# Performance work log

Measured on AMD Instinct MI355X. Metric: run time of the kernel, lower is better.

## Reference

```python
import jax, jax.numpy as jnp
import numpy as np

NUM_EMBEDDINGS = 16384
EMBED_DIM = 256
COMMITMENT_COST = 0.25  # legacy=True: vq_loss = commit + beta * codebook


def setup_inputs() -> dict:
    key = jax.random.key(0)
    k1, k2, k3, k4 = jax.random.split(key, 4)
    z = jax.random.normal(k1, (8, 2048, EMBED_DIM), dtype=jnp.float32)
    # frozen codebook: normal(0, embedding_dim ** -0.5)
    codebook = jax.random.normal(k2, (NUM_EMBEDDINGS, EMBED_DIM), dtype=jnp.float32) * (EMBED_DIM ** -0.5)
    # learnable linear projection, torch default uniform init
    bound = 1.0 / np.sqrt(EMBED_DIM)
    proj_w = jax.random.uniform(k3, (EMBED_DIM, EMBED_DIM), dtype=jnp.float32, minval=-bound, maxval=bound)
    proj_b = jax.random.uniform(k4, (EMBED_DIM,), dtype=jnp.float32, minval=-bound, maxval=bound)
    return {"z": z, "codebook": codebook, "proj_w": proj_w, "proj_b": proj_b}


def reference(z, codebook, proj_w, proj_b):
    B, T, D = z.shape
    # projected codebook (the only learned part of the quantizer)
    quant_codebook = codebook @ proj_w.T + proj_b  # [K, D]
    z_flat = z.reshape(-1, D)  # [N, D]
    # squared L2 distances: ||z||^2 + ||c||^2 - 2 z.c
    dists = (
        jnp.sum(z_flat * z_flat, axis=1, keepdims=True)
        + jnp.sum(quant_codebook * quant_codebook, axis=1)
        - 2.0 * jnp.einsum("nd,kd->nk", z_flat, quant_codebook)
    )  # [N, K]
    idx = jnp.argmin(dists, axis=1)  # [N]
    quantized = quant_codebook[idx].reshape(z.shape)  # [B, T, D]

    commitment_loss = jnp.mean((jax.lax.stop_gradient(quantized) - z) ** 2)
    codebook_loss = jnp.mean((quantized - jax.lax.stop_gradient(z)) ** 2)
    vq_loss = commitment_loss + COMMITMENT_COST * codebook_loss  # legacy formulation

    # straight-through estimator
    quantized = z + jax.lax.stop_gradient(quantized - z)
    encoding_indices = idx.reshape(B, T)
    return quantized, vq_loss, encoding_indices
```

## Files before the change

### kernel.cpp

```cpp
#include <hip/hip_runtime.h>

typedef unsigned short u16;
typedef __bf16 bf16x8 __attribute__((ext_vector_type(8)));
typedef float f32x4 __attribute__((ext_vector_type(4)));

#define NQ 16384
#define NC 16384
#define DD 256
#define BM 256
#define BN 256
#define BK 32
#define NSPLIT 8
#define NPART (NSPLIT * 2)
#define NTILES ((NC / NSPLIT) / BN)
#define NSTEPS (NTILES * 8)

__device__ __forceinline__ u16 f2bf(float x) {
  unsigned u = __float_as_uint(x);
  u += 0x7fffu + ((u >> 16) & 1u);
  return (u16)(u >> 16);
}
__device__ __forceinline__ float bf2f(u16 h) {
  return __uint_as_float(((unsigned)h) << 16);
}

__device__ __forceinline__ void gl2lds16(const void* g, void* l) {
  __builtin_amdgcn_global_load_lds((__attribute__((address_space(1))) void*)g,
                                   (__attribute__((address_space(3))) void*)l,
                                   16, 0, 0);
}

#define MFMA_AGPR(ACC, A, B) \
  asm("v_mfma_f32_16x16x32_bf16 %0, %1, %2, %0" : "+a"(ACC) : "v"(A), "v"(B))

__global__ __launch_bounds__(256) void split_z_kernel(const float* __restrict__ z,
                                                      u16* __restrict__ Ah,
                                                      u16* __restrict__ Al) {
  size_t i = (size_t)blockIdx.x * 256 + threadIdx.x;
  float4 v = ((const float4*)z)[i];
  float f[4] = {v.x, v.y, v.z, v.w};
  u16 hh[4], ll[4];
#pragma unroll
  for (int j = 0; j < 4; ++j) {
    hh[j] = f2bf(f[j]);
    ll[j] = f2bf(f[j] - bf2f(hh[j]));
  }
  ushort4 h; h.x = hh[0]; h.y = hh[1]; h.z = hh[2]; h.w = hh[3];
  ushort4 l; l.x = ll[0]; l.y = ll[1]; l.z = ll[2]; l.w = ll[3];
  ((ushort4*)Ah)[i] = h;
  ((ushort4*)Al)[i] = l;
}

__global__ __launch_bounds__(256) void norm_both_kernel(const float* __restrict__ z,
                                                        const float* __restrict__ qc,
                                                        float* __restrict__ zn,
                                                        float* __restrict__ cn) {
  const int t = threadIdx.x;
  const int j = t & 7;
  const bool isq = blockIdx.x >= (NQ / 32);
  const int b = isq ? (blockIdx.x - NQ / 32) : blockIdx.x;
  const float* x = isq ? qc : z;
  float* nrm = isq ? cn : zn;
  const int row = b * 32 + (t >> 3);
  const float* q = x + (size_t)row * 256;
  float half[2];
#pragma unroll
  for (int h = 0; h < 2; ++h) {
    const float* p = q + h * 128;
    float v0 = p[j];
    float r = __fmul_rn(v0, v0);
#pragma unroll
    for (int i = 8; i < 128; i += 8) {
      float v = p[i + j];
      r = __fadd_rn(r, __fmul_rn(v, v));
    }
    float s1 = __fadd_rn(r, __shfl_xor(r, 1));
    float s2 = __fadd_rn(s1, __shfl_xor(s1, 2));
    half[h] = __fadd_rn(s2, __shfl_xor(s2, 4));
  }
  if (j == 0) nrm[row] = __fadd_rn(half[0], half[1]);
}

__global__ __launch_bounds__(256) void qc_gemm_kernel(const float* __restrict__ cb,
                                                      const float* __restrict__ W,
                                                      const float* __restrict__ bias,
                                                      float* __restrict__ qc,
                                                      u16* __restrict__ Bh,
                                                      u16* __restrict__ Bl) {
  __shared__ float As[64][33];
  __shared__ float Bs[64][33];
  const int bm = blockIdx.x >> 2;
  const int bn = blockIdx.x & 3;
  const int m0 = bm * 64, n0 = bn * 64;
  const int t = threadIdx.x;
  const int tx = t & 15, ty = t >> 4;
  float acc[4][4] = {};
  for (int kc = 0; kc < 256; kc += 32) {
    __syncthreads();
#pragma unroll
    for (int j = 0; j < 8; ++j) {
      int idx = j * 256 + t;
      int r = idx >> 5, c = idx & 31;
      As[r][c] = cb[(size_t)(m0 + r) * 256 + kc + c];
      Bs[r][c] = W[(size_t)(n0 + r) * 256 + kc + c];
    }
    __syncthreads();
#pragma unroll
    for (int kk = 0; kk < 32; ++kk) {
      float a[4], b[4];
#pragma unroll
      for (int u = 0; u < 4; ++u) a[u] = As[ty * 4 + u][kk];
#pragma unroll
      for (int v = 0; v < 4; ++v) b[v] = Bs[tx * 4 + v][kk];
#pragma unroll
      for (int u = 0; u < 4; ++u)
#pragma unroll
        for (int v = 0; v < 4; ++v) acc[u][v] += a[u] * b[v];
    }
  }
#pragma unroll
  for (int u = 0; u < 4; ++u) {
    const int r = m0 + ty * 4 + u;
    const int c0 = n0 + tx * 4;
    float q4[4];
#pragma unroll
    for (int v = 0; v < 4; ++v) q4[v] = acc[u][v] + bias[c0 + v];
    float4 qv; qv.x = q4[0]; qv.y = q4[1]; qv.z = q4[2]; qv.w = q4[3];
    *(float4*)&qc[(size_t)r * 256 + c0] = qv;
    u16 hh[4], ll[4];
#pragma unroll
    for (int v = 0; v < 4; ++v) {
      hh[v] = f2bf(q4[v]);
      ll[v] = f2bf(q4[v] - bf2f(hh[v]));
    }
    ushort4 h; h.x = hh[0]; h.y = hh[1]; h.z = hh[2]; h.w = hh[3];
    ushort4 l; l.x = ll[0]; l.y = ll[1]; l.z = ll[2]; l.w = ll[3];
    *(ushort4*)&Bh[(size_t)r * 256 + c0] = h;
    *(ushort4*)&Bl[(size_t)r * 256 + c0] = l;
  }
}

__global__ __launch_bounds__(512, 2) void vq_argmin_kernel(
    const u16* __restrict__ Ah, const u16* __restrict__ Al,
    const u16* __restrict__ Bh, const u16* __restrict__ Bl,
    const float* __restrict__ cnorm, const float* __restrict__ znorm,
    float* __restrict__ pval, int* __restrict__ pidx) {
  __shared__ __align__(16) u16 Ahs[2][BM * BK];
  __shared__ __align__(16) u16 Als[2][BM * BK];
  __shared__ __align__(16) u16 Bhs[2][BN * BK];
  __shared__ __align__(16) u16 Bls[2][BN * BK];

  const int bm = blockIdx.x / NSPLIT;
  const int spl = blockIdx.x % NSPLIT;
  const int lane = threadIdx.x & 63;
  const int wid = threadIdx.x >> 6;
  const int wm = wid >> 1, wn = wid & 1;
  const int l15 = lane & 15;
  const int lg = lane >> 4;
  const int m0 = bm * BM;
  const int ns0 = spl * (NC / NSPLIT);

  const int st_r = lane >> 2;
  const int st_k = (((lane & 3) ^ ((lane >> 3) & 3)) << 3);

  const int rd_sw = ((lg ^ ((l15 >> 1) & 3)) << 3);

  const int grp0 = wid * 2, grp1 = wid * 2 + 1;
  const int stoff0 = (grp0 * 16 + st_r) * DD + st_k;
  const int stoff1 = (grp1 * 16 + st_r) * DD + st_k;
  const int dst0 = grp0 * 512, dst1 = grp1 * 512;

  auto stage = [&](int buf, int s2) {
    const int kcc = (s2 & 7) * BK;
    const u16* pAh = Ah + (size_t)m0 * DD + kcc;
    const u16* pAl = Al + (size_t)m0 * DD + kcc;
    const size_t bb = (size_t)(ns0 + (s2 >> 3) * BN) * DD + kcc;
    const u16* pBh = Bh + bb;
    const u16* pBl = Bl + bb;
    gl2lds16(pAh + stoff0, &Ahs[buf][dst0]);
    gl2lds16(pAl + stoff0, &Als[buf][dst0]);
    gl2lds16(pBh + stoff0, &Bhs[buf][dst0]);
    gl2lds16(pBl + stoff0, &Bls[buf][dst0]);
    gl2lds16(pAh + stoff1, &Ahs[buf][dst1]);
    gl2lds16(pAl + stoff1, &Als[buf][dst1]);
    gl2lds16(pBh + stoff1, &Bhs[buf][dst1]);
    gl2lds16(pBl + stoff1, &Bls[buf][dst1]);
  };

  float rmin[4][4];
  int ridx[4][4];
#pragma unroll
  for (int a = 0; a < 4; ++a)
#pragma unroll
    for (int b = 0; b < 4; ++b) { rmin[a][b] = 3.4e38f; ridx[a][b] = 0; }

  stage(0, 0);
  asm volatile("s_waitcnt vmcnt(0)" ::: "memory");
  __builtin_amdgcn_s_barrier();

  for (int nt = 0; nt < NTILES; ++nt) {
    const int n0 = ns0 + nt * BN;
    f32x4 acc[4][8];
#pragma unroll
    for (int a = 0; a < 4; ++a)
#pragma unroll
      for (int b = 0; b < 8; ++b) {
        f32x4 zz = {0.f, 0.f, 0.f, 0.f};
        acc[a][b] = zz;
      }

#pragma unroll 1
    for (int k8 = 0; k8 < 8; ++k8) {
      const int s = nt * 8 + k8;
      const int cur = s & 1;

      __builtin_amdgcn_s_barrier();
      if (s + 1 < NSTEPS) {
        stage(cur ^ 1, s + 1);
        asm volatile("s_waitcnt vmcnt(8)" ::: "memory");
      } else {
        asm volatile("s_waitcnt vmcnt(0)" ::: "memory");
      }
      __builtin_amdgcn_s_barrier();
      __builtin_amdgcn_sched_barrier(0);

      bf16x8 ah[4], al[4];
#pragma unroll
      for (int mi = 0; mi < 4; ++mi) {
        const int r = wm * 64 + mi * 16 + l15;
        const int off = r * BK + rd_sw;
        ah[mi] = *(const bf16x8*)&Ahs[cur][off];
        al[mi] = *(const bf16x8*)&Als[cur][off];
      }
      __builtin_amdgcn_s_setprio(1);
      {
        bf16x8 bh[4], bl[4];
#pragma unroll
        for (int nq = 0; nq < 4; ++nq) {
          const int r = wn * 128 + nq * 16 + l15;
          const int off = r * BK + rd_sw;
          bh[nq] = *(const bf16x8*)&Bhs[cur][off];
          bl[nq] = *(const bf16x8*)&Bls[cur][off];
        }
#pragma unroll
        for (int nq = 0; nq < 4; ++nq)
#pragma unroll
          for (int mi = 0; mi < 4; ++mi)
            MFMA_AGPR(acc[mi][nq], ah[mi], bh[nq]);
#pragma unroll
        for (int nq = 0; nq < 4; ++nq)
#pragma unroll
          for (int mi = 0; mi < 4; ++mi)
            MFMA_AGPR(acc[mi][nq], ah[mi], bl[nq]);
#pragma unroll
        for (int nq = 0; nq < 4; ++nq)
#pragma unroll
          for (int mi = 0; mi < 4; ++mi)
            MFMA_AGPR(acc[mi][nq], al[mi], bh[nq]);
      }
      __builtin_amdgcn_sched_barrier(0);
      {
        bf16x8 bh[4], bl[4];
#pragma unroll
        for (int nq = 0; nq < 4; ++nq) {
          const int r = wn * 128 + (4 + nq) * 16 + l15;
          const int off = r * BK + rd_sw;
          bh[nq] = *(const bf16x8*)&Bhs[cur][off];
          bl[nq] = *(const bf16x8*)&Bls[cur][off];
        }
#pragma unroll
        for (int nq = 0; nq < 4; ++nq)
#pragma unroll
          for (int mi = 0; mi < 4; ++mi)
            MFMA_AGPR(acc[mi][4 + nq], ah[mi], bh[nq]);
#pragma unroll
        for (int nq = 0; nq < 4; ++nq)
#pragma unroll
          for (int mi = 0; mi < 4; ++mi)
            MFMA_AGPR(acc[mi][4 + nq], ah[mi], bl[nq]);
#pragma unroll
        for (int nq = 0; nq < 4; ++nq)
#pragma unroll
          for (int mi = 0; mi < 4; ++mi)
            MFMA_AGPR(acc[mi][4 + nq], al[mi], bh[nq]);
      }
      __builtin_amdgcn_s_setprio(0);
    }

    float cnv[8];
#pragma unroll
    for (int ni = 0; ni < 8; ++ni)
      cnv[ni] = cnorm[n0 + wn * 128 + ni * 16 + l15];
#pragma unroll
    for (int mi = 0; mi < 4; ++mi) {
      float zr[4];
#pragma unroll
      for (int i = 0; i < 4; ++i)
        zr[i] = znorm[m0 + wm * 64 + mi * 16 + lg * 4 + i];
#pragma unroll
      for (int ni = 0; ni < 8; ++ni) {
        const int col = n0 + wn * 128 + ni * 16 + l15;
        const float cn = cnv[ni];
#pragma unroll
        for (int i = 0; i < 4; ++i) {
          const float s = __fadd_rn(zr[i], cn);
          const float v = __fsub_rn(s, __fmul_rn(2.0f, acc[mi][ni][i]));
          if (v < rmin[mi][i]) { rmin[mi][i] = v; ridx[mi][i] = col; }
        }
      }
    }
  }
#pragma unroll
  for (int mi = 0; mi < 4; ++mi)
#pragma unroll
    for (int i = 0; i < 4; ++i) {
      float v = rmin[mi][i];
      int ix = ridx[mi][i];
#pragma unroll
      for (int d = 1; d < 16; d <<= 1) {
        float ov = __shfl_xor(v, d);
        int oi = __shfl_xor(ix, d);
        if (ov < v || (ov == v && oi < ix)) { v = ov; ix = oi; }
      }
      if (l15 == 0) {
        const int row = m0 + wm * 64 + mi * 16 + lg * 4 + i;
        const int part = spl * 2 + wn;
        pval[(size_t)part * NQ + row] = v;
        pidx[(size_t)part * NQ + row] = ix;
      }
    }
}

__global__ __launch_bounds__(256) void finalize_kernel(
    const float* __restrict__ pval, const int* __restrict__ pidx,
    const float* __restrict__ qc, const float* __restrict__ z,
    float* __restrict__ out, float* __restrict__ loss_acc) {
  __shared__ int sidx[8];
  __shared__ float red[256];
  const int bid = blockIdx.x;
  const int t = threadIdx.x;
  if (t < 8) {
    const int row = bid * 8 + t;
    float best = pval[row];
    int bi = pidx[row];
    for (int s2 = 1; s2 < NPART; ++s2) {
      float v = pval[(size_t)s2 * NQ + row];
      int ix = pidx[(size_t)s2 * NQ + row];
      if (v < best || (v == best && ix < bi)) { best = v; bi = ix; }
    }
    sidx[t] = bi;
    out[4194305 + row] = (float)bi;
  }
  __syncthreads();
  float d2 = 0.f;
#pragma unroll
  for (int r = 0; r < 8; ++r) {
    const int row = bid * 8 + r;
    const int ix = sidx[r];
    const float q = qc[(size_t)ix * 256 + t];
    const float zz = z[(size_t)row * 256 + t];
    out[(size_t)row * 256 + t] = q;
    const float d = q - zz;
    d2 += d * d;
  }
  red[t] = d2;
  for (int st = 128; st; st >>= 1) {
    __syncthreads();
    if (t < st) red[t] += red[t + st];
  }
  if (t == 0) atomicAdd(loss_acc, red[0]);
}

__global__ void write_loss_kernel(const float* __restrict__ loss_acc, float* __restrict__ out) {
  out[4194304] = 1.25f * loss_acc[0] / 4194304.0f;
}

extern "C" void kernel_launch(void* const* d_in, const int* in_sizes, int n_in,
                              void* d_out, int out_size, void* d_ws, size_t ws_size,
                              hipStream_t stream) {
  const float* z = (const float*)d_in[0];
  const float* cb = (const float*)d_in[1];
  const float* W = (const float*)d_in[2];
  const float* bias = (const float*)d_in[3];
  float* out = (float*)d_out;
  char* ws = (char*)d_ws;

  constexpr size_t OFF_QC = 0;
  constexpr size_t OFF_AH = OFF_QC + 16777216;
  constexpr size_t OFF_AL = OFF_AH + 8388608;
  constexpr size_t OFF_BH = OFF_AL + 8388608;
  constexpr size_t OFF_BL = OFF_BH + 8388608;
  constexpr size_t OFF_CN = OFF_BL + 8388608;
  constexpr size_t OFF_ZN = OFF_CN + 65536;
  constexpr size_t OFF_PV = OFF_ZN + 65536;
  constexpr size_t OFF_PI = OFF_PV + 1048576;
  constexpr size_t OFF_ACC = OFF_PI + 1048576;

  float* qc = (float*)(ws + OFF_QC);
  u16* Ah = (u16*)(ws + OFF_AH);
  u16* Al = (u16*)(ws + OFF_AL);
  u16* Bh = (u16*)(ws + OFF_BH);
  u16* Bl = (u16*)(ws + OFF_BL);
  float* cn = (float*)(ws + OFF_CN);
  float* zn = (float*)(ws + OFF_ZN);
  float* pv = (float*)(ws + OFF_PV);
  int* pi = (int*)(ws + OFF_PI);
  float* lacc = (float*)(ws + OFF_ACC);

  hipMemsetAsync(lacc, 0, 4, stream);
  split_z_kernel<<<4096, 256, 0, stream>>>(z, Ah, Al);
  qc_gemm_kernel<<<1024, 256, 0, stream>>>(cb, W, bias, qc, Bh, Bl);
  norm_both_kernel<<<NQ / 32 + NC / 32, 256, 0, stream>>>(z, qc, zn, cn);
  vq_argmin_kernel<<<(NQ / BM) * NSPLIT, 512, 0, stream>>>(Ah, Al, Bh, Bl, cn, zn, pv, pi);
  finalize_kernel<<<NQ / 8, 256, 0, stream>>>(pv, pi, qc, z, out, lacc);
  write_loss_kernel<<<1, 1, 0, stream>>>(lacc, out);
}
```

Before: 522.8 us.

## Fuse z split with z-norm and enlarge codebook projection GEMM tiles

Merges the z bf16 hi/lo split with the z row-norm computation: z is staged in shared memory and read once from global memory instead of twice. The codebook projection GEMM moves from 64x64 tiles with 4x4 per-thread outputs to 128x128 tiles with 8x8 per-thread outputs and transposed LDS layout, so it can use vectorized float4 shared loads and do more arithmetic per load. The larger tile uses more registers and launches only 256 blocks, which may reduce occupancy. These preprocessing kernels are small next to the main argmin kernel.

```diff
diff --git a/kernel.cpp b/kernel.cpp
--- a/kernel.cpp
+++ b/kernel.cpp
@@ -33,35 +33,58 @@
 #define MFMA_AGPR(ACC, A, B) \
   asm("v_mfma_f32_16x16x32_bf16 %0, %1, %2, %0" : "+a"(ACC) : "v"(A), "v"(B))
 
-__global__ __launch_bounds__(256) void split_z_kernel(const float* __restrict__ z,
-                                                      u16* __restrict__ Ah,
-                                                      u16* __restrict__ Al) {
-  size_t i = (size_t)blockIdx.x * 256 + threadIdx.x;
-  float4 v = ((const float4*)z)[i];
-  float f[4] = {v.x, v.y, v.z, v.w};
-  u16 hh[4], ll[4];
-#pragma unroll
-  for (int j = 0; j < 4; ++j) {
-    hh[j] = f2bf(f[j]);
-    ll[j] = f2bf(f[j] - bf2f(hh[j]));
-  }
-  ushort4 h; h.x = hh[0]; h.y = hh[1]; h.z = hh[2]; h.w = hh[3];
-  ushort4 l; l.x = ll[0]; l.y = ll[1]; l.z = ll[2]; l.w = ll[3];
-  ((ushort4*)Ah)[i] = h;
-  ((ushort4*)Al)[i] = l;
-}
-
-__global__ __launch_bounds__(256) void norm_both_kernel(const float* __restrict__ z,
-                                                        const float* __restrict__ qc,
-                                                        float* __restrict__ zn,
-                                                        float* __restrict__ cn) {
+__global__ __launch_bounds__(256) void split_z_norm_kernel(const float* __restrict__ z,
+                                                           u16* __restrict__ Ah,
+                                                           u16* __restrict__ Al,
+                                                           float* __restrict__ zn) {
+  __shared__ float zs[32 * 256];
+  const int t = threadIdx.x;
+#pragma unroll
+  for (int j = 0; j < 8; ++j) {
+    const int loc = j * 256 + t;
+    const size_t i = (size_t)blockIdx.x * 2048 + loc;
+    float4 v = ((const float4*)z)[i];
+    *(float4*)&zs[loc * 4] = v;
+    float f[4] = {v.x, v.y, v.z, v.w};
+    u16 hh[4], ll[4];
+#pragma unroll
+    for (int q = 0; q < 4; ++q) {
+      hh[q] = f2bf(f[q]);
+      ll[q] = f2bf(f[q] - bf2f(hh[q]));
+    }
+    ushort4 h; h.x = hh[0]; h.y = hh[1]; h.z = hh[2]; h.w = hh[3];
+    ushort4 l; l.x = ll[0]; l.y = ll[1]; l.z = ll[2]; l.w = ll[3];
+    ((ushort4*)Ah)[i] = h;
+    ((ushort4*)Al)[i] = l;
+  }
+  __syncthreads();
+  const int j = t & 7;
+  const int lrow = t >> 3;
+  const int row = blockIdx.x * 32 + lrow;
+  const float* q = zs + lrow * 256;
+  float half[2];
+#pragma unroll
+  for (int h = 0; h < 2; ++h) {
+    const float* p = q + h * 128;
+    float v0 = p[j];
+    float r = __fmul_rn(v0, v0);
+#pragma unroll
+    for (int i = 8; i < 128; i += 8) {
+      float v = p[i + j];
+      r = __fadd_rn(r, __fmul_rn(v, v));
+    }
+    float s1 = __fadd_rn(r, __shfl_xor(r, 1));
+    float s2 = __fadd_rn(s1, __shfl_xor(s1, 2));
+    half[h] = __fadd_rn(s2, __shfl_xor(s2, 4));
+  }
+  if (j == 0) zn[row] = __fadd_rn(half[0], half[1]);
+}
+
+__global__ __launch_bounds__(256) void norm256_kernel(const float* __restrict__ x,
+                                                      float* __restrict__ nrm) {
   const int t = threadIdx.x;
   const int j = t & 7;
-  const bool isq = blockIdx.x >= (NQ / 32);
-  const int b = isq ? (blockIdx.x - NQ / 32) : blockIdx.x;
-  const float* x = isq ? qc : z;
-  float* nrm = isq ? cn : zn;
-  const int row = b * 32 + (t >> 3);
+  const int row = blockIdx.x * 32 + (t >> 3);
   const float* q = x + (size_t)row * 256;
   float half[2];
 #pragma unroll
@@ -87,56 +110,60 @@
                                                       float* __restrict__ qc,
                                                       u16* __restrict__ Bh,
                                                       u16* __restrict__ Bl) {
-  __shared__ float As[64][33];
-  __shared__ float Bs[64][33];
-  const int bm = blockIdx.x >> 2;
-  const int bn = blockIdx.x & 3;
-  const int m0 = bm * 64, n0 = bn * 64;
+  __shared__ float At[32][132];
+  __shared__ float Bt[32][132];
+  const int bm = blockIdx.x >> 1;
+  const int bn = blockIdx.x & 1;
+  const int m0 = bm * 128, n0 = bn * 128;
   const int t = threadIdx.x;
   const int tx = t & 15, ty = t >> 4;
-  float acc[4][4] = {};
+  float acc[8][8] = {};
   for (int kc = 0; kc < 256; kc += 32) {
     __syncthreads();
 #pragma unroll
-    for (int j = 0; j < 8; ++j) {
-      int idx = j * 256 + t;
-      int r = idx >> 5, c = idx & 31;
-      As[r][c] = cb[(size_t)(m0 + r) * 256 + kc + c];
-      Bs[r][c] = W[(size_t)(n0 + r) * 256 + kc + c];
+    for (int j = 0; j < 16; ++j) {
+      const int idx = j * 256 + t;
+      const int r = idx >> 5, c = idx & 31;
+      At[c][r] = cb[(size_t)(m0 + r) * 256 + kc + c];
+      Bt[c][r] = W[(size_t)(n0 + r) * 256 + kc + c];
     }
     __syncthreads();
 #pragma unroll
     for (int kk = 0; kk < 32; ++kk) {
-      float a[4], b[4];
-#pragma unroll
-      for (int u = 0; u < 4; ++u) a[u] = As[ty * 4 + u][kk];
-#pragma unroll
-      for (int v = 0; v < 4; ++v) b[v] = Bs[tx * 4 + v][kk];
-#pragma unroll
-      for (int u = 0; u < 4; ++u)
-#pragma unroll
-        for (int v = 0; v < 4; ++v) acc[u][v] += a[u] * b[v];
-    }
-  }
-#pragma unroll
-  for (int u = 0; u < 4; ++u) {
-    const int r = m0 + ty * 4 + u;
-    const int c0 = n0 + tx * 4;
-    float q4[4];
-#pragma unroll
-    for (int v = 0; v < 4; ++v) q4[v] = acc[u][v] + bias[c0 + v];
-    float4 qv; qv.x = q4[0]; qv.y = q4[1]; qv.z = q4[2]; qv.w = q4[3];
-    *(float4*)&qc[(size_t)r * 256 + c0] = qv;
-    u16 hh[4], ll[4];
-#pragma unroll
-    for (int v = 0; v < 4; ++v) {
-      hh[v] = f2bf(q4[v]);
-      ll[v] = f2bf(q4[v] - bf2f(hh[v]));
-    }
-    ushort4 h; h.x = hh[0]; h.y = hh[1]; h.z = hh[2]; h.w = hh[3];
-    ushort4 l; l.x = ll[0]; l.y = ll[1]; l.z = ll[2]; l.w = ll[3];
-    *(ushort4*)&Bh[(size_t)r * 256 + c0] = h;
-    *(ushort4*)&Bl[(size_t)r * 256 + c0] = l;
+      float4 a0 = *(const float4*)&At[kk][ty * 8];
+      float4 a1 = *(const float4*)&At[kk][ty * 8 + 4];
+      float4 b0 = *(const float4*)&Bt[kk][tx * 8];
+      float4 b1 = *(const float4*)&Bt[kk][tx * 8 + 4];
+      float a[8] = {a0.x, a0.y, a0.z, a0.w, a1.x, a1.y, a1.z, a1.w};
+      float b[8] = {b0.x, b0.y, b0.z, b0.w, b1.x, b1.y, b1.z, b1.w};
+#pragma unroll
+      for (int u = 0; u < 8; ++u)
+#pragma unroll
+        for (int v = 0; v < 8; ++v) acc[u][v] += a[u] * b[v];
+    }
+  }
+#pragma unroll
+  for (int u = 0; u < 8; ++u) {
+    const int r = m0 + ty * 8 + u;
+#pragma unroll
+    for (int g = 0; g < 2; ++g) {
+      const int c0 = n0 + tx * 8 + g * 4;
+      float q4[4];
+#pragma unroll
+      for (int v = 0; v < 4; ++v) q4[v] = acc[u][g * 4 + v] + bias[c0 + v];
+      float4 qv; qv.x = q4[0]; qv.y = q4[1]; qv.z = q4[2]; qv.w = q4[3];
+      *(float4*)&qc[(size_t)r * 256 + c0] = qv;
+      u16 hh[4], ll[4];
+#pragma unroll
+      for (int v = 0; v < 4; ++v) {
+        hh[v] = f2bf(q4[v]);
+        ll[v] = f2bf(q4[v] - bf2f(hh[v]));
+      }
+      ushort4 h; h.x = hh[0]; h.y = hh[1]; h.z = hh[2]; h.w = hh[3];
+      ushort4 l; l.x = ll[0]; l.y = ll[1]; l.z = ll[2]; l.w = ll[3];
+      *(ushort4*)&Bh[(size_t)r * 256 + c0] = h;
+      *(ushort4*)&Bl[(size_t)r * 256 + c0] = l;
+    }
   }
 }
 
@@ -408,9 +435,9 @@
   float* lacc = (float*)(ws + OFF_ACC);
 
   hipMemsetAsync(lacc, 0, 4, stream);
-  split_z_kernel<<<4096, 256, 0, stream>>>(z, Ah, Al);
-  qc_gemm_kernel<<<1024, 256, 0, stream>>>(cb, W, bias, qc, Bh, Bl);
-  norm_both_kernel<<<NQ / 32 + NC / 32, 256, 0, stream>>>(z, qc, zn, cn);
+  split_z_norm_kernel<<<NQ / 32, 256, 0, stream>>>(z, Ah, Al, zn);
+  qc_gemm_kernel<<<256, 256, 0, stream>>>(cb, W, bias, qc, Bh, Bl);
+  norm256_kernel<<<NC / 32, 256, 0, stream>>>(qc, cn);
   vq_argmin_kernel<<<(NQ / BM) * NSPLIT, 512, 0, stream>>>(Ah, Al, Bh, Bl, cn, zn, pv, pi);
   finalize_kernel<<<NQ / 8, 256, 0, stream>>>(pv, pi, qc, z, out, lacc);
   write_loss_kernel<<<1, 1, 0, stream>>>(lacc, out);
```

New measurement: 507.8 us. -2.9%, faster.
